# Kernel optimization log

Measured on AMD Instinct MI355X. Metric: run time of the kernel, lower is better.

The kernel has to match this reference:

```python
import jax, jax.numpy as jnp
import numpy as np

B, C, H, W = 16, 512, 64, 64
CB, CG = 64, 256  # bottleneck = C/8, g = C/2


def _conv1x1(x, w, b):
    # x: [B,Cin,H,W], w: [Cout,Cin] -> [B,Cout,H,W]
    return jnp.einsum('bchw,oc->bohw', x, w) + b[None, :, None, None]


def _avg_pool2(x):
    # 2x2 average pool, stride 2. x: [B,C,H,W] with even H,W.
    b, c, h, w = x.shape
    return x.reshape(b, c, h // 2, 2, w // 2, 2).mean(axis=(3, 5))


def setup_inputs() -> dict:
    key = jax.random.key(0)
    ks = jax.random.split(key, 6)
    s = 0.02
    return {
        'x': jax.random.normal(ks[0], (B, C, H, W), jnp.float32),
        'w_theta': jax.random.normal(ks[1], (CB, C), jnp.float32) * s,
        'b_theta': jnp.zeros((CB,), jnp.float32),
        'w_phi': jax.random.normal(ks[2], (CB, C), jnp.float32) * s,
        'b_phi': jnp.zeros((CB,), jnp.float32),
        'w_g': jax.random.normal(ks[3], (CG, C), jnp.float32) * s,
        'b_g': jnp.zeros((CG,), jnp.float32),
        'w_out': jax.random.normal(ks[4], (C, CG), jnp.float32) * s,
        'b_out': jnp.zeros((C,), jnp.float32),
        'gamma': jnp.zeros((1,), jnp.float32),
    }


def reference(x, w_theta, b_theta, w_phi, b_phi, w_g, b_g, w_out, b_out, gamma):
    b, c, h, w = x.shape
    n = h * w          # query locations
    m = n // 4         # pooled key/value locations

    theta = _conv1x1(x, w_theta, b_theta).reshape(b, CB, n)           # [B,CB,N]
    phi = _avg_pool2(_conv1x1(x, w_phi, b_phi)).reshape(b, CB, m)     # [B,CB,M]
    g = _avg_pool2(_conv1x1(x, w_g, b_g)).reshape(b, CG, m)           # [B,CG,M]

    logits = jnp.einsum('bcn,bcm->bnm', theta, phi)                   # [B,N,M]
    attn = jax.nn.softmax(logits, axis=-1)
    out = jnp.einsum('bcm,bnm->bcn', g, attn).reshape(b, CG, h, w)    # [B,CG,H,W]
    out = _conv1x1(out, w_out, b_out)                                 # [B,C,H,W]
    return gamma[0] * out + x
```

## Files before the change

kernel.cpp:

```cpp
#include <hip/hip_runtime.h>
#include <math.h>


typedef unsigned short u16;
typedef short bf16x8 __attribute__((ext_vector_type(8)));
typedef float f32x16 __attribute__((ext_vector_type(16)));
typedef u16 u16x4 __attribute__((ext_vector_type(4)));
typedef int i32x4 __attribute__((ext_vector_type(4)));

#define MFMA32 __builtin_amdgcn_mfma_f32_32x32x16_bf16
#define B_ 16
#define C_ 512
#define N_ 4096
#define M_ 1024
#define LOG2E 1.44269504088896f
#define FIXMAX 8.0f

__device__ __forceinline__ u16 f2b(float f) {
  unsigned u = __float_as_uint(f);
  return (u16)((u + 0x7FFFu + ((u >> 16) & 1u)) >> 16);
}
__device__ __forceinline__ unsigned cvtpk(float a, float b) {
  unsigned r;
  asm("v_cvt_pk_bf16_f32 %0, %1, %2" : "=v"(r) : "v"(a), "v"(b));
  return r;
}
__device__ __forceinline__ void permswap(unsigned &a, unsigned &b) {
  asm("v_permlane32_swap_b32 %0, %1" : "+v"(a), "+v"(b));
}
__device__ __forceinline__ float exp2v(float a) {
  float r;
  asm("v_exp_f32 %0, %1" : "=v"(r) : "v"(a));
  return r;
}
__device__ __forceinline__ f32x16 fz16() {
  f32x16 z;
#pragma unroll
  for (int i = 0; i < 16; ++i) z[i] = 0.0f;
  return z;
}


__global__ __launch_bounds__(256) void cvt_all_kernel(
    const float* __restrict__ w_theta, const float* __restrict__ w_phi,
    const float* __restrict__ w_g, const float* __restrict__ w_out,
    const float* __restrict__ gamma, u16* __restrict__ dth, u16* __restrict__ dph,
    u16* __restrict__ dg, u16* __restrict__ dwo) {
  int i = blockIdx.x * 256 + threadIdx.x;
  if (i < 16384) {
    const float* s = (i < 8192) ? w_theta : w_phi;
    u16* d = (i < 8192) ? dth : dph;
    float scale = (i < 8192) ? LOG2E : 1.0f;
    int j = i & 8191;
    int o = j >> 7, c = (j & 127) * 4;
    float4 vv = *(const float4*)(s + (size_t)o * 512 + c);
    int idx = (((o >> 5) * 8 + (c >> 6)) * 4 + ((c >> 4) & 3)) * 512 +
              (((c >> 3) & 1) * 32 + (o & 31)) * 8 + (c & 7);
    u16x4 ot = {f2b(vv.x * scale), f2b(vv.y * scale), f2b(vv.z * scale), f2b(vv.w * scale)};
    *(u16x4*)(d + idx) = ot;
  } else if (i < 49152) {
    int j = i - 16384;
    int o = j >> 7, c = (j & 127) * 4;
    float4 vv = *(const float4*)(w_g + (size_t)o * 512 + c);
    int idx = (((o >> 5) * 8 + (c >> 6)) * 4 + ((c >> 4) & 3)) * 512 +
              (((c >> 3) & 1) * 32 + (o & 31)) * 8 + (c & 7);
    u16x4 ot = {f2b(vv.x), f2b(vv.y), f2b(vv.z), f2b(vv.w)};
    *(u16x4*)(dg + idx) = ot;
  } else {
    int j = i - 49152;
    int o = j >> 6, k = (j & 63) * 4;
    float scale = gamma[0];
    float4 vv = *(const float4*)(w_out + (size_t)o * 256 + k);
    int idx = ((o >> 5) * 16 + (k >> 4)) * 512 +
              (((k >> 3) & 1) * 32 + (o & 31)) * 8 + (k & 7);
    u16x4 ot = {f2b(vv.x * scale), f2b(vv.y * scale), f2b(vv.z * scale), f2b(vv.w * scale)};
    *(u16x4*)(dwo + idx) = ot;
  }
}

__global__ __launch_bounds__(512) void prep_kernel(
    const float* __restrict__ x, const u16* __restrict__ wth,
    const u16* __restrict__ wph, const u16* __restrict__ wg,
    const float* __restrict__ bth, const float* __restrict__ bph,
    const float* __restrict__ bg, u16* __restrict__ th, u16* __restrict__ ph,
    u16* __restrict__ vt) {
  __shared__ u16 xb[128 * 68];
  __shared__ u16 xpt[32 * 68];
  const int t = threadIdx.x;
  const int w = t >> 6, l = t & 63, lo = l & 31, hi = l >> 5;
  const int nb = blockIdx.x, b = blockIdx.y;
  const int n0 = nb * 128;
  const int lcol = (t & 31) * 4;
  const int lrow = t >> 5;

  f32x16 acc0 = fz16(), acc1 = fz16(), a_ph = fz16();

  float v[16];
  auto loadv = [&](int c0) {
#pragma unroll
    for (int i = 0; i < 4; ++i) {
      float4 f = *(const float4*)(x + ((size_t)(b * C_ + c0 + lrow + 16 * i)) * N_ + n0 + lcol);
      v[4*i] = f.x; v[4*i+1] = f.y; v[4*i+2] = f.z; v[4*i+3] = f.w;
    }
  };
  auto writeT = [&]() {
#pragma unroll
    for (int i = 0; i < 4; ++i) {
      int c = lrow + 16 * i;
      int blk = c >> 3;
#pragma unroll
      for (int k = 0; k < 4; ++k) {
        int n = lcol + k;
        int swz = ((n >> 2) ^ (n >> 5)) & 7;
        xb[n * 68 + ((blk ^ swz) * 8) + (c & 7)] = f2b(v[4*i+k]);
      }
    }
    float pA[4], pB[4];
#pragma unroll
    for (int i = 0; i < 4; ++i) {
      pA[i] = v[4*i] + v[4*i+1];
      pB[i] = v[4*i+2] + v[4*i+3];
    }
#pragma unroll
    for (int i = 0; i < 4; ++i) {
      pA[i] += __shfl_xor(pA[i], 16, 64);
      pB[i] += __shfl_xor(pB[i], 16, 64);
    }
    if ((t & 31) < 16) {
      int m0 = (t & 31) * 2;
#pragma unroll
      for (int i = 0; i < 4; ++i) {
        int c = lrow + 16 * i;
        xpt[m0 * 68 + c] = f2b(0.25f * pA[i]);
        xpt[(m0 + 1) * 68 + c] = f2b(0.25f * pB[i]);
      }
    }
  };
  auto domfma = [&](int c0b) {
    if (w < 4) {
      const int n = 32 * w + lo;
      const int rbase = n * 68;
      const int nswz = ((n >> 2) ^ (n >> 5)) & 7;
#pragma unroll
      for (int kh = 0; kh < 4; ++kh) {
        bf16x8 xa = *(const bf16x8*)(&xb[rbase + (((2*kh + hi) ^ nswz) * 8)]);
        bf16x8 w0 = *(const bf16x8*)(wth + ((c0b) * 4 + kh) * 512 + l * 8);
        bf16x8 w1 = *(const bf16x8*)(wth + ((8 + c0b) * 4 + kh) * 512 + l * 8);
        acc0 = MFMA32(xa, w0, acc0, 0, 0, 0);
        acc1 = MFMA32(xa, w1, acc1, 0, 0, 0);
      }
    } else {
      const int wg4 = w - 4;
      const u16* xpw = &xpt[lo * 68];
#pragma unroll
      for (int kh = 0; kh < 4; ++kh) {
        bf16x8 xp8 = *(const bf16x8*)(xpw + kh * 16 + hi * 8);
        bf16x8 g0 = *(const bf16x8*)(wg + ((16*wg4 + c0b) * 4 + kh) * 512 + l * 8);
        bf16x8 g1 = *(const bf16x8*)(wg + ((16*wg4 + 8 + c0b) * 4 + kh) * 512 + l * 8);
        acc0 = MFMA32(g0, xp8, acc0, 0, 0, 0);
        acc1 = MFMA32(g1, xp8, acc1, 0, 0, 0);
        if (wg4 < 2) {
          bf16x8 wp8 = *(const bf16x8*)(wph + ((wg4*8 + c0b) * 4 + kh) * 512 + l * 8);
          a_ph = MFMA32(xp8, wp8, a_ph, 0, 0, 0);
        }
      }
    }
  };

  loadv(0);
  for (int i = 0; i < 8; ++i) {
    if (i) __syncthreads();
    writeT();
    if (i < 7) loadv((i + 1) * 64);
    __syncthreads();
    domfma(i);
  }

  int rr[16];
#pragma unroll
  for (int r = 0; r < 16; ++r) rr[r] = (r & 3) + 8 * (r >> 2) + 4 * hi;

  if (w < 4) {
    u16* thb = th + (size_t)b * 262144;
#pragma unroll
    for (int r = 0; r < 16; ++r) {
      int sub = (((lo >> 3) & 1) * 32 + rr[r]) * 8 + (lo & 7);
      thb[((nb*4 + w)*4 + (lo >> 4)) * 512 + sub]     = f2b(acc0[r] + LOG2E * bth[lo]);
      thb[((nb*4 + w)*4 + 2 + (lo >> 4)) * 512 + sub] = f2b(acc1[r] + LOG2E * bth[32 + lo]);
    }
  } else {
    const int wg4 = w - 4;
    u16* vtb = vt + (size_t)b * 262144;
#pragma unroll
    for (int r = 0; r < 16; ++r) {
      int cg0 = 64 * wg4 + rr[r];
      int sub = (((lo >> 3) & 1) * 32 + rr[r]) * 8 + (lo & 7);
      int kk = (nb & 1) * 2 + (lo >> 4);
      vtb[(((nb >> 1) * 8 + 2*wg4) * 4 + kk) * 512 + sub]     = f2b(acc0[r] + bg[cg0]);
      vtb[(((nb >> 1) * 8 + 2*wg4 + 1) * 4 + kk) * 512 + sub] = f2b(acc1[r] + bg[cg0 + 32]);
    }
    if (wg4 < 2) {
      u16* phb = ph + (size_t)b * 65536;
#pragma unroll
      for (int r = 0; r < 16; ++r) {
        int sub = (((lo >> 3) & 1) * 32 + rr[r]) * 8 + (lo & 7);
        phb[(nb*4 + 2*wg4 + (lo >> 4)) * 512 + sub] = f2b(a_ph[r] + bph[32*wg4 + lo]);
      }
    }
  }
}

__global__ __launch_bounds__(256, 3) void attn_kernel(
    const u16* __restrict__ th, const u16* __restrict__ ph,
    const u16* __restrict__ vt, const u16* __restrict__ wo,
    const float* __restrict__ b_out, const float* __restrict__ gamma,
    const float* __restrict__ x, float* __restrict__ out) {
  __shared__ u16 Os[16384];

  const int t = threadIdx.x;
  const int w = t >> 6, l = t & 63, lo = l & 31, hi = l >> 5;
  const int p = w & 1, h = w >> 1;
  const int flat = blockIdx.y * 64 + blockIdx.x;
  const int nf = (flat & 7) * 128 + (flat >> 3);
  const int b = nf >> 6, nb6 = nf & 63;
  const int qp = nb6 * 64 + 32 * p;
  const int jq = nb6 * 2 + p;

  const u16* thb = th + (size_t)b * 262144;
  const u16* phb = ph + (size_t)b * 65536;
  const u16* vtb = vt + (size_t)b * 262144;

  bf16x8 thB[4];
#pragma unroll
  for (int kh = 0; kh < 4; ++kh)
    thB[kh] = *(const bf16x8*)(thb + (jq * 4 + kh) * 512 + l * 8);

  f32x16 acc[4];
#pragma unroll
  for (int ct = 0; ct < 4; ++ct) acc[ct] = fz16();
  float sp[4] = {0.0f, 0.0f, 0.0f, 0.0f};

  for (int jm = 0; jm < 32; ++jm) {
    bf16x8 pf[4];
#pragma unroll
    for (int kh = 0; kh < 4; ++kh)
      pf[kh] = *(const bf16x8*)(phb + (jm * 4 + kh) * 512 + l * 8);
    f32x16 S = fz16();
#pragma unroll
    for (int kh = 0; kh < 4; ++kh) S = MFMA32(pf[kh], thB[kh], S, 0, 0, 0);

#pragma unroll
    for (int i = 0; i < 16; ++i) {
      S[i] = exp2v(S[i] - FIXMAX);
      sp[i & 3] += S[i];
    }

    bf16x8 Pf[2];
#pragma unroll
    for (int s = 0; s < 2; ++s) {
      unsigned a0 = cvtpk(S[8*s+0], S[8*s+1]);
      unsigned a1 = cvtpk(S[8*s+2], S[8*s+3]);
      unsigned a2 = cvtpk(S[8*s+4], S[8*s+5]);
      unsigned a3 = cvtpk(S[8*s+6], S[8*s+7]);
      permswap(a0, a2);
      permswap(a1, a3);
      i32x4 wv = {(int)a0, (int)a1, (int)a2, (int)a3};
      Pf[s] = __builtin_bit_cast(bf16x8, wv);
    }

    const int ic = jm >> 1, kh0 = (jm & 1) * 2;
    __builtin_amdgcn_s_setprio(1);
#pragma unroll
    for (int ct2 = 0; ct2 < 4; ++ct2) {
      const u16* vp = vtb + ((ic * 8 + 4 * h + ct2) * 4 + kh0) * 512 + l * 8;
      bf16x8 vf0 = *(const bf16x8*)(vp);
      bf16x8 vf1 = *(const bf16x8*)(vp + 512);
      acc[ct2] = MFMA32(vf0, Pf[0], acc[ct2], 0, 0, 0);
      acc[ct2] = MFMA32(vf1, Pf[1], acc[ct2], 0, 0, 0);
    }
    __builtin_amdgcn_s_setprio(0);
  }

  float lsum = (sp[0] + sp[1]) + (sp[2] + sp[3]);
  lsum += __shfl_xor(lsum, 32, 64);
  const float linv = 1.0f / lsum;

  u16* osp = Os + p * 8192;
#pragma unroll
  for (int ct2 = 0; ct2 < 4; ++ct2) {
    f32x16& A = acc[ct2];
#pragma unroll
    for (int s = 0; s < 2; ++s) {
      unsigned a0 = cvtpk(A[8*s+0]*linv, A[8*s+1]*linv);
      unsigned a1 = cvtpk(A[8*s+2]*linv, A[8*s+3]*linv);
      unsigned a2 = cvtpk(A[8*s+4]*linv, A[8*s+5]*linv);
      unsigned a3 = cvtpk(A[8*s+6]*linv, A[8*s+7]*linv);
      permswap(a0, a2);
      permswap(a1, a3);
      i32x4 wv = {(int)a0, (int)a1, (int)a2, (int)a3};
      int f = 8 * h + 2 * ct2 + s;
      int blk8 = 2 * f + hi;
      *(bf16x8*)(osp + lo * 256 + ((blk8 ^ (lo & 7)) * 8)) =
          __builtin_bit_cast(bf16x8, wv);
    }
  }
  __syncthreads();

  bf16x8 Of[16];
#pragma unroll
  for (int f = 0; f < 16; ++f)
    Of[f] = *(const bf16x8*)(osp + lo * 256 + (((2 * f + hi) ^ (lo & 7)) * 8));

  int rr[16];
#pragma unroll
  for (int r = 0; r < 16; ++r) rr[r] = (r & 3) + 8 * (r >> 2) + 4 * hi;

  const float gamma0 = gamma[0];
  for (int ctc = 0; ctc < 8; ++ctc) {
    f32x16 facc = fz16();
    const u16* wp = wo + (size_t)((8 * h + ctc) * 16) * 512 + l * 8;
#pragma unroll
    for (int f = 0; f < 16; ++f) {
      bf16x8 wfr = *(const bf16x8*)(wp + f * 512);
      facc = MFMA32(wfr, Of[f], facc, 0, 0, 0);
    }
#pragma unroll
    for (int r = 0; r < 16; ++r) {
      int c = 256 * h + 32 * ctc + rr[r];
      size_t idx = ((size_t)(b * C_ + c)) * N_ + qp + lo;
      float xv = __builtin_nontemporal_load(&x[idx]);
      __builtin_nontemporal_store(facc[r] + gamma0 * b_out[c] + xv, &out[idx]);
    }
  }
}

extern "C" void kernel_launch(void* const* d_in, const int* in_sizes, int n_in,
                              void* d_out, int out_size, void* d_ws, size_t ws_size,
                              hipStream_t stream) {
  (void)in_sizes; (void)n_in; (void)out_size; (void)ws_size;
  const float* x       = (const float*)d_in[0];
  const float* w_theta = (const float*)d_in[1];
  const float* b_theta = (const float*)d_in[2];
  const float* w_phi   = (const float*)d_in[3];
  const float* b_phi   = (const float*)d_in[4];
  const float* w_g     = (const float*)d_in[5];
  const float* b_g     = (const float*)d_in[6];
  const float* w_out   = (const float*)d_in[7];
  const float* b_out   = (const float*)d_in[8];
  const float* gamma   = (const float*)d_in[9];
  float* out = (float*)d_out;

  char* ws = (char*)d_ws;
  u16* th  = (u16*)(ws);
  u16* ph  = (u16*)(ws + 8388608);
  u16* vt  = (u16*)(ws + 10485760);
  u16* wth = (u16*)(ws + 18874368);
  u16* wph = (u16*)(ws + 18939904);
  u16* wg  = (u16*)(ws + 19005440);
  u16* wo  = (u16*)(ws + 19267584);

  cvt_all_kernel<<<320, 256, 0, stream>>>(w_theta, w_phi, w_g, w_out, gamma,
                                          wth, wph, wg, wo);
  prep_kernel<<<dim3(32, 16), 512, 0, stream>>>(x, wth, wph, wg, b_theta, b_phi,
                                                b_g, th, ph, vt);
  attn_kernel<<<dim3(64, 16), 256, 0, stream>>>(th, ph, vt, wo, b_out, gamma, x, out);
}
```

Baseline: 198.2 us.

## Double-buffer phi/V tiles in LDS via async global_load_lds with bigger blocks

The attention kernel now uses 512-thread blocks covering 128 query rows, and stages each key/value chunk (V tile plus phi tile) cooperatively into double-buffered LDS through direct global-to-LDS async copies. Each chunk is loaded once per block and shared across the waves, instead of every wave streaming phi and V from global memory itself, and the next chunk's load overlaps compute on the current one. The cost is 80KB of LDS per block and block-wide barriers every iteration, which limits occupancy. The epilogue code not shown here also has to be correct for the new 8-wave layout.

```diff
diff --git a/kernel.cpp b/kernel.cpp
--- a/kernel.cpp
+++ b/kernel.cpp
@@ -32,6 +32,11 @@
   float r;
   asm("v_exp_f32 %0, %1" : "=v"(r) : "v"(a));
   return r;
+}
+__device__ __forceinline__ void async_cp16(u16* lds, const u16* g) {
+  __builtin_amdgcn_global_load_lds(
+      (const __attribute__((address_space(1))) unsigned int*)g,
+      (__attribute__((address_space(3))) unsigned int*)lds, 16, 0, 0);
 }
 __device__ __forceinline__ f32x16 fz16() {
   f32x16 z;
@@ -210,21 +215,20 @@
   }
 }
 
-__global__ __launch_bounds__(256, 3) void attn_kernel(
+__global__ __launch_bounds__(512, 4) void attn_kernel(
     const u16* __restrict__ th, const u16* __restrict__ ph,
     const u16* __restrict__ vt, const u16* __restrict__ wo,
     const float* __restrict__ b_out, const float* __restrict__ gamma,
     const float* __restrict__ x, float* __restrict__ out) {
-  __shared__ u16 Os[16384];
+  __shared__ u16 smem[40960];
 
   const int t = threadIdx.x;
   const int w = t >> 6, l = t & 63, lo = l & 31, hi = l >> 5;
-  const int p = w & 1, h = w >> 1;
-  const int flat = blockIdx.y * 64 + blockIdx.x;
-  const int nf = (flat & 7) * 128 + (flat >> 3);
-  const int b = nf >> 6, nb6 = nf & 63;
-  const int qp = nb6 * 64 + 32 * p;
-  const int jq = nb6 * 2 + p;
+  const int p = w & 3, h = w >> 2;
+  const int flat = blockIdx.y * 32 + blockIdx.x;
+  const int nf = (flat & 7) * 64 + (flat >> 3);
+  const int b = nf >> 5, nb5 = nf & 31;
+  const int qp = nb5 * 128 + 32 * p;
 
   const u16* thb = th + (size_t)b * 262144;
   const u16* phb = ph + (size_t)b * 65536;
@@ -233,59 +237,90 @@
   bf16x8 thB[4];
 #pragma unroll
   for (int kh = 0; kh < 4; ++kh)
-    thB[kh] = *(const bf16x8*)(thb + (jq * 4 + kh) * 512 + l * 8);
+    thB[kh] = *(const bf16x8*)(thb + ((nb5 * 4 + p) * 4 + kh) * 512 + l * 8);
 
   f32x16 acc[4];
 #pragma unroll
   for (int ct = 0; ct < 4; ++ct) acc[ct] = fz16();
   float sp[4] = {0.0f, 0.0f, 0.0f, 0.0f};
 
-  for (int jm = 0; jm < 32; ++jm) {
-    bf16x8 pf[4];
-#pragma unroll
-    for (int kh = 0; kh < 4; ++kh)
-      pf[kh] = *(const bf16x8*)(phb + (jm * 4 + kh) * 512 + l * 8);
-    f32x16 S = fz16();
-#pragma unroll
-    for (int kh = 0; kh < 4; ++kh) S = MFMA32(pf[kh], thB[kh], S, 0, 0, 0);
-
-#pragma unroll
-    for (int i = 0; i < 16; ++i) {
-      S[i] = exp2v(S[i] - FIXMAX);
-      sp[i & 3] += S[i];
-    }
-
-    bf16x8 Pf[2];
-#pragma unroll
-    for (int s = 0; s < 2; ++s) {
-      unsigned a0 = cvtpk(S[8*s+0], S[8*s+1]);
-      unsigned a1 = cvtpk(S[8*s+2], S[8*s+3]);
-      unsigned a2 = cvtpk(S[8*s+4], S[8*s+5]);
-      unsigned a3 = cvtpk(S[8*s+6], S[8*s+7]);
-      permswap(a0, a2);
-      permswap(a1, a3);
-      i32x4 wv = {(int)a0, (int)a1, (int)a2, (int)a3};
-      Pf[s] = __builtin_bit_cast(bf16x8, wv);
-    }
-
-    const int ic = jm >> 1, kh0 = (jm & 1) * 2;
-    __builtin_amdgcn_s_setprio(1);
-#pragma unroll
-    for (int ct2 = 0; ct2 < 4; ++ct2) {
-      const u16* vp = vtb + ((ic * 8 + 4 * h + ct2) * 4 + kh0) * 512 + l * 8;
-      bf16x8 vf0 = *(const bf16x8*)(vp);
-      bf16x8 vf1 = *(const bf16x8*)(vp + 512);
-      acc[ct2] = MFMA32(vf0, Pf[0], acc[ct2], 0, 0, 0);
-      acc[ct2] = MFMA32(vf1, Pf[1], acc[ct2], 0, 0, 0);
-    }
-    __builtin_amdgcn_s_setprio(0);
+  auto stage = [&](int nbuf, int ic) {
+    const int offu = w * 2560;
+#pragma unroll
+    for (int i = 0; i < 5; ++i) {
+      int o = offu + i * 512;
+      u16* dst = &smem[nbuf * 20480 + o];
+      const u16* src = (o < 16384) ? (vtb + (size_t)ic * 16384 + o + l * 8)
+                                   : (phb + (size_t)ic * 4096 + (o - 16384) + l * 8);
+      async_cp16(dst, src);
+    }
+  };
+
+  stage(0, 0);
+  asm volatile("s_waitcnt vmcnt(0)" ::: "memory");
+  __builtin_amdgcn_sched_barrier(0);
+  __builtin_amdgcn_s_barrier();
+
+  int buf = 0;
+  for (int ic = 0; ic < 16; ++ic) {
+    if (ic < 15) stage(buf ^ 1, ic + 1);
+
+    const u16* Vs = &smem[buf * 20480];
+    const u16* Ps = Vs + 16384;
+#pragma unroll
+    for (int jml = 0; jml < 2; ++jml) {
+      bf16x8 pf[4];
+#pragma unroll
+      for (int kh = 0; kh < 4; ++kh)
+        pf[kh] = *(const bf16x8*)(Ps + (jml * 4 + kh) * 512 + l * 8);
+      f32x16 S = fz16();
+#pragma unroll
+      for (int kh = 0; kh < 4; ++kh) S = MFMA32(pf[kh], thB[kh], S, 0, 0, 0);
+
+#pragma unroll
+      for (int i = 0; i < 16; ++i) {
+        S[i] = exp2v(S[i] - FIXMAX);
+        sp[i & 3] += S[i];
+      }
+
+      bf16x8 Pf[2];
+#pragma unroll
+      for (int s = 0; s < 2; ++s) {
+        unsigned a0 = cvtpk(S[8*s+0], S[8*s+1]);
+        unsigned a1 = cvtpk(S[8*s+2], S[8*s+3]);
+        unsigned a2 = cvtpk(S[8*s+4], S[8*s+5]);
+        unsigned a3 = cvtpk(S[8*s+6], S[8*s+7]);
+        permswap(a0, a2);
+        permswap(a1, a3);
+        i32x4 wv = {(int)a0, (int)a1, (int)a2, (int)a3};
+        Pf[s] = __builtin_bit_cast(bf16x8, wv);
+      }
+
+      __builtin_amdgcn_s_setprio(1);
+#pragma unroll
+      for (int ct2 = 0; ct2 < 4; ++ct2) {
+        const u16* vp = Vs + ((4 * h + ct2) * 4 + jml * 2) * 512 + l * 8;
+        bf16x8 vf0 = *(const bf16x8*)(vp);
+        bf16x8 vf1 = *(const bf16x8*)(vp + 512);
+        acc[ct2] = MFMA32(vf0, Pf[0], acc[ct2], 0, 0, 0);
+        acc[ct2] = MFMA32(vf1, Pf[1], acc[ct2], 0, 0, 0);
+      }
+      __builtin_amdgcn_s_setprio(0);
+    }
+
+    asm volatile("s_waitcnt vmcnt(0)" ::: "memory");
+    __builtin_amdgcn_sched_barrier(0);
+    __builtin_amdgcn_s_barrier();
+    buf ^= 1;
   }
 
   float lsum = (sp[0] + sp[1]) + (sp[2] + sp[3]);
   lsum += __shfl_xor(lsum, 32, 64);
   const float linv = 1.0f / lsum;
 
-  u16* osp = Os + p * 8192;
+  __builtin_amdgcn_s_barrier();
+
+  u16* osp = smem + p * 8192;
 #pragma unroll
   for (int ct2 = 0; ct2 < 4; ++ct2) {
     f32x16& A = acc[ct2];
@@ -363,5 +398,5 @@
                                           wth, wph, wg, wo);
   prep_kernel<<<dim3(32, 16), 512, 0, stream>>>(x, wth, wph, wg, b_theta, b_phi,
                                                 b_g, th, ph, vt);
-  attn_kernel<<<dim3(64, 16), 256, 0, stream>>>(th, ph, vt, wo, b_out, gamma, x, out);
-}
+  attn_kernel<<<dim3(32, 16), 512, 0, stream>>>(th, ph, vt, wo, b_out, gamma, x, out);
+}
```

Result: faster. 193.8 us (-2.2%).
